# Kernel tuning notes

Hardware: AMD Instinct MI355X
Metric: run time of the kernel (lower is better)

Reference implementation:

```python
import jax, jax.numpy as jnp
import numpy as np

B, A, C = 64, 8732, 81


def setup_inputs() -> dict:
    key = jax.random.key(0)
    k1, k2, k3, k4, k5 = jax.random.split(key, 5)
    scores = jax.random.normal(k1, (B, A, C), dtype=jnp.float32)
    boxes = jax.random.normal(k2, (B, A, 4), dtype=jnp.float32)
    gt_labels = jax.random.randint(k3, (B, A), 0, C)
    gt_boxes = jax.random.normal(k4, (B, A, 4), dtype=jnp.float32)
    mask = jax.random.uniform(k5, (B, A)) < 0.02
    return {"scores": scores, "boxes": boxes, "gt_labels": gt_labels,
            "gt_boxes": gt_boxes, "mask": mask}


def reference(scores, boxes, gt_labels, gt_boxes, mask):
    dtype = scores.dtype
    maskf = mask.astype(dtype)
    pos_num = mask.sum(axis=-1, keepdims=True)          # [B,1] per-image positives
    N = jnp.maximum(1, mask.sum()).astype(dtype)        # max(1, total positives)

    # localization: smooth L1 (beta=1) summed over positive anchors
    d = boxes - gt_boxes
    ad = jnp.abs(d)
    sl1 = jnp.where(ad < 1.0, 0.5 * d * d, ad - 0.5)    # [B,A,4]
    loc_loss = (sl1.sum(axis=-1) * maskf).sum() / N

    # per-anchor cross entropy
    logp = jax.nn.log_softmax(scores, axis=-1)          # [B,A,C]
    c_loss = -jnp.take_along_axis(logp, gt_labels[..., None], axis=-1)[..., 0]  # [B,A]

    # hard negative mining: zero positives, rank by descending loss, keep top 3*pos_num
    conf_neg = jnp.where(mask, jnp.zeros((), dtype), c_loss)
    conf_idx = jnp.argsort(-conf_neg, axis=-1)          # descending sort indices
    rank = jnp.argsort(conf_idx, axis=-1)               # rank of each anchor
    neg_mask = rank < 3 * pos_num                       # [B,A]

    conf_loss = ((c_loss * maskf).sum() + (c_loss * neg_mask.astype(dtype)).sum()) / N
    total_loss = loc_loss + conf_loss
    return total_loss, loc_loss, conf_loss
```

## Files before the change

### kernel.cpp

```cpp
#include <hip/hip_runtime.h>
#include <math.h>

#define NB 64
#define NA 8732
#define NC 81
#define TOTAL (NB * NA)
#define APB 128
#define TPB 512
#define NBLK (TOTAL / APB)


__device__ __forceinline__ float quadsum(float x) {
    x += __int_as_float(__builtin_amdgcn_update_dpp(
        0, __float_as_int(x), 0xB1, 0xF, 0xF, true));
    x += __int_as_float(__builtin_amdgcn_update_dpp(
        0, __float_as_int(x), 0x4E, 0xF, 0xF, true));
    return x;
}

__device__ __forceinline__ void gload_lds16(const float4* g, float4* l) {
    __builtin_amdgcn_global_load_lds(
        (const __attribute__((address_space(1))) unsigned int*)g,
        (__attribute__((address_space(3))) unsigned int*)l,
        16, 0, 0);
}

__global__ __launch_bounds__(TPB) void main_kernel(
    const float* __restrict__ scores, const float* __restrict__ boxes,
    const int* __restrict__ gt_labels, const float* __restrict__ gt_boxes,
    const int* __restrict__ mask, float* __restrict__ conf_neg,
    float* __restrict__ block_loc, float* __restrict__ block_pcs)
{
    __shared__ float lds[APB * NC];
    __shared__ float wredl[8], wredp[8];
    const int tid  = threadIdx.x;
    const int lane = tid & 63;
    const int wid  = tid >> 6;
    const int base = blockIdx.x * APB;

    const float4* __restrict__ src = (const float4*)(scores + (size_t)base * NC);
    float4* dst = (float4*)lds;
    gload_lds16(src + tid,        dst + tid);
    gload_lds16(src + tid +  512, dst + tid +  512);
    gload_lds16(src + tid + 1024, dst + tid + 1024);
    gload_lds16(src + tid + 1536, dst + tid + 1536);
    gload_lds16(src + tid + 2048, dst + tid + 2048);
    if (tid < 32) gload_lds16(src + tid + 2560, dst + tid + 2560);

    float loc = 0.0f;
    if (tid < APB) {
        const int a = base + tid;
        if (mask[a]) {
            const float4 bx = *(const float4*)(boxes    + (size_t)a * 4);
            const float4 gb = *(const float4*)(gt_boxes + (size_t)a * 4);
            const float d0 = bx.x - gb.x, d1 = bx.y - gb.y;
            const float d2 = bx.z - gb.z, d3 = bx.w - gb.w;
            const float a0 = fabsf(d0), a1 = fabsf(d1), a2 = fabsf(d2), a3 = fabsf(d3);
            loc = (a0 < 1.f ? 0.5f * d0 * d0 : a0 - 0.5f)
                + (a1 < 1.f ? 0.5f * d1 * d1 : a1 - 0.5f)
                + (a2 < 1.f ? 0.5f * d2 * d2 : a2 - 0.5f)
                + (a3 < 1.f ? 0.5f * d3 * d3 : a3 - 0.5f);
        }
    }
    __syncthreads();

    const int al = tid >> 2;
    const int q  = tid & 3;
    const float* __restrict__ row = lds + al * NC;
    float e = 0.0f;
    #pragma unroll
    for (int j = 0; j < 20; ++j) e += __expf(row[q * 20 + j]);
    if (q == 3) e += __expf(row[80]);
    e = quadsum(e);

    float pcs = 0.0f;
    if (q == 0) {
        const int a = base + al;
        const int lab = gt_labels[a];
        const float c = __logf(e) - row[lab];
        const int m = mask[a];
        conf_neg[a] = m ? 0.f : c;
        pcs = m ? c : 0.f;
    }

    #pragma unroll
    for (int o = 32; o; o >>= 1) {
        loc += __shfl_down(loc, o);
        pcs += __shfl_down(pcs, o);
    }
    if (lane == 0) { wredl[wid] = loc; wredp[wid] = pcs; }
    __syncthreads();
    if (tid == 0) {
        float sl = 0.f, sp = 0.f;
        #pragma unroll
        for (int w = 0; w < 8; ++w) { sl += wredl[w]; sp += wredp[w]; }
        block_loc[blockIdx.x] = sl;
        block_pcs[blockIdx.x] = sp;
    }
}

__global__ __launch_bounds__(1024) void topk_kernel(
    const float* __restrict__ conf_neg, const int* __restrict__ mask,
    int* __restrict__ pos_count, float* __restrict__ accv)
{
    __shared__ unsigned sv[NA];
    __shared__ __align__(16) int whist[64][256];
    __shared__ int hist4[4][256];
    __shared__ int   redi[16];
    __shared__ float redf[16];
    __shared__ unsigned spfx;
    __shared__ int skr;
    __shared__ int sk;
    const int tid  = threadIdx.x;
    const int lane = tid & 63;
    const int wid  = tid >> 6;
    const int hid  = tid >> 4;
    const int b = blockIdx.x;
    const float* __restrict__ row  = conf_neg + (size_t)b * NA;
    const int*   __restrict__ mrow = mask     + (size_t)b * NA;

    int myc = 0;
    for (int i = tid; i < NA; i += 1024) {
        sv[i] = __float_as_uint(row[i]);
        myc += mrow[i];
    }
    #pragma unroll
    for (int o = 32; o; o >>= 1) myc += __shfl_down(myc, o);
    if (lane == 0) redi[wid] = myc;
    __syncthreads();
    if (tid == 0) {
        int p = 0;
        #pragma unroll
        for (int w = 0; w < 16; ++w) p += redi[w];
        pos_count[b] = p;
        int kk = 3 * p;
        if (kk > NA) kk = NA;
        sk = kk;
    }
    __syncthreads();
    int k = sk;
    if (k <= 0) {
        if (tid == 0) accv[b] = 0.0f;
        return;
    }

    unsigned prefix = 0u;
    int kr = k;
    for (int shift = 24; shift >= 0; shift -= 8) {
        int4* w4 = (int4*)whist;
        const int4 z = make_int4(0, 0, 0, 0);
        w4[tid] = z; w4[tid + 1024] = z; w4[tid + 2048] = z; w4[tid + 3072] = z;
        __syncthreads();

        const unsigned himask = (shift == 24) ? 0u : (0xFFFFFFFFu << (shift + 8));
        for (int i = tid; i < NA; i += 1024) {
            const unsigned v = sv[i];
            if ((v & himask) == prefix)
                atomicAdd(&whist[hid][(v >> shift) & 255], 1);
        }
        __syncthreads();

        {
            const int p = tid >> 8;
            const int bb = tid & 255;
            int s = 0;
            #pragma unroll
            for (int w = 0; w < 16; ++w) s += whist[(p << 4) + w][bb];
            hist4[p][bb] = s;
        }
        __syncthreads();

        if (wid == 0) {
            int h0, h1, h2, h3;
            {
                const int b0i = 4 * lane;
                h0 = hist4[0][b0i]     + hist4[1][b0i]     + hist4[2][b0i]     + hist4[3][b0i];
                h1 = hist4[0][b0i + 1] + hist4[1][b0i + 1] + hist4[2][b0i + 1] + hist4[3][b0i + 1];
                h2 = hist4[0][b0i + 2] + hist4[1][b0i + 2] + hist4[2][b0i + 2] + hist4[3][b0i + 2];
                h3 = hist4[0][b0i + 3] + hist4[1][b0i + 3] + hist4[2][b0i + 3] + hist4[3][b0i + 3];
            }
            const int s3 = h3, s2 = h2 + s3, s1 = h1 + s2, s0 = h0 + s1;
            int incl = s0;
            #pragma unroll
            for (int off = 1; off < 64; off <<= 1) {
                const int v = __shfl_down(incl, off);
                if (lane + off < 64) incl += v;
            }
            const int E = incl - s0;
            const int S0 = E + s0, S1 = E + s1, S2 = E + s2, S3 = E + s3;
            if (S0 >= kr && S1 < kr) { spfx = prefix | ((unsigned)(4 * lane)     << shift); skr = kr - S1; }
            else if (S1 >= kr && S2 < kr) { spfx = prefix | ((unsigned)(4 * lane + 1) << shift); skr = kr - S2; }
            else if (S2 >= kr && S3 < kr) { spfx = prefix | ((unsigned)(4 * lane + 2) << shift); skr = kr - S3; }
            else if (S3 >= kr && E  < kr) { spfx = prefix | ((unsigned)(4 * lane + 3) << shift); skr = kr - E;  }
        }
        __syncthreads();
        prefix = spfx;
        kr = skr;
    }

    float s = 0.0f; int cg = 0;
    for (int i = tid; i < NA; i += 1024) {
        const unsigned u = sv[i];
        if (u > prefix) { s += __uint_as_float(u); cg++; }
    }
    #pragma unroll
    for (int o = 32; o; o >>= 1) { s += __shfl_down(s, o); cg += __shfl_down(cg, o); }
    if ((tid & 63) == 0) { redf[wid] = s; redi[wid] = cg; }
    __syncthreads();
    if (tid == 0) {
        float ts = 0.f; int tc = 0;
        #pragma unroll
        for (int w = 0; w < 16; ++w) { ts += redf[w]; tc += redi[w]; }
        ts += (float)(k - tc) * __uint_as_float(prefix);
        accv[b] = ts;
    }
}

__global__ __launch_bounds__(1024) void final_kernel(
    const float* __restrict__ block_loc, const float* __restrict__ block_pcs,
    const int* __restrict__ pos_count, const float* __restrict__ accv,
    float* __restrict__ out)
{
    __shared__ float rl[16], rp[16];
    const int tid = threadIdx.x;
    const int wid = tid >> 6;
    float sl = 0.f, sp = 0.f;
    for (int i = tid; i < NBLK; i += 1024) { sl += block_loc[i]; sp += block_pcs[i]; }
    int   p  = (tid < NB) ? pos_count[tid] : 0;
    float sa = (tid < NB) ? accv[tid]      : 0.f;
    #pragma unroll
    for (int o = 32; o; o >>= 1) {
        sl += __shfl_down(sl, o);
        sp += __shfl_down(sp, o);
        p  += __shfl_down(p, o);
        sa += __shfl_down(sa, o);
    }
    if ((tid & 63) == 0) { rl[wid] = sl; rp[wid] = sp; }
    __syncthreads();
    if (tid == 0) {
        float tl = 0.f, tp = 0.f;
        #pragma unroll
        for (int w = 0; w < 16; ++w) { tl += rl[w]; tp += rp[w]; }
        const float N = fmaxf(1.0f, (float)p);
        const float loc  = tl / N;
        const float conf = (tp + sa) / N;
        out[0] = loc + conf;
        out[1] = loc;
        out[2] = conf;
    }
}

extern "C" void kernel_launch(void* const* d_in, const int* in_sizes, int n_in,
                              void* d_out, int out_size, void* d_ws, size_t ws_size,
                              hipStream_t stream) {
    const float* scores    = (const float*)d_in[0];
    const float* boxes     = (const float*)d_in[1];
    const int*   gt_labels = (const int*)d_in[2];
    const float* gt_boxes  = (const float*)d_in[3];
    const int*   mask      = (const int*)d_in[4];
    float* out = (float*)d_out;

    float* conf_neg  = (float*)d_ws;
    int*   pos_count = (int*)(conf_neg + TOTAL);
    float* accv      = (float*)(pos_count + NB);
    float* block_loc = accv + NB;
    float* block_pcs = block_loc + NBLK;

    hipLaunchKernelGGL(main_kernel, dim3(NBLK), dim3(TPB), 0, stream,
                       scores, boxes, gt_labels, gt_boxes, mask,
                       conf_neg, block_loc, block_pcs);
    hipLaunchKernelGGL(topk_kernel, dim3(NB), dim3(1024), 0, stream,
                       conf_neg, mask, pos_count, accv);
    hipLaunchKernelGGL(final_kernel, dim3(1), dim3(1024), 0, stream,
                       block_loc, block_pcs, pos_count, accv, out);
}
```

Before: 284.0 us.

## Fuse final reduction into topk via last-block counter and halve main tile

Removes the separate final_kernel launch. The last topk block to finish, detected with an atomic counter that main_kernel resets, now does the global reduction and writes the outputs. Also halves the anchors per block in main_kernel (64 anchors, 256 threads) with an occupancy hint of 7 blocks per CU, to raise concurrency in the memory-bound scores pass. This adds an atomic and threadfences, and the 7-block hint may constrain registers.

```diff
diff --git a/kernel.cpp b/kernel.cpp
--- a/kernel.cpp
+++ b/kernel.cpp
@@ -5,8 +5,8 @@
 #define NA 8732
 #define NC 81
 #define TOTAL (NB * NA)
-#define APB 128
-#define TPB 512
+#define APB 64
+#define TPB 256
 #define NBLK (TOTAL / APB)
 
 
@@ -25,27 +25,30 @@
         16, 0, 0);
 }
 
-__global__ __launch_bounds__(TPB) void main_kernel(
+__global__ __launch_bounds__(TPB, 7) void main_kernel(
     const float* __restrict__ scores, const float* __restrict__ boxes,
     const int* __restrict__ gt_labels, const float* __restrict__ gt_boxes,
     const int* __restrict__ mask, float* __restrict__ conf_neg,
-    float* __restrict__ block_loc, float* __restrict__ block_pcs)
+    float* __restrict__ block_loc, float* __restrict__ block_pcs,
+    int* __restrict__ done)
 {
-    __shared__ float lds[APB * NC];
-    __shared__ float wredl[8], wredp[8];
+    __shared__ float lds[APB * NC + 256];
+    __shared__ float wredl[4], wredp[4];
     const int tid  = threadIdx.x;
     const int lane = tid & 63;
     const int wid  = tid >> 6;
     const int base = blockIdx.x * APB;
 
+    if (blockIdx.x == 0 && tid == 0) *done = 0;
+
     const float4* __restrict__ src = (const float4*)(scores + (size_t)base * NC);
     float4* dst = (float4*)lds;
     gload_lds16(src + tid,        dst + tid);
+    gload_lds16(src + tid +  256, dst + tid +  256);
     gload_lds16(src + tid +  512, dst + tid +  512);
+    gload_lds16(src + tid +  768, dst + tid +  768);
     gload_lds16(src + tid + 1024, dst + tid + 1024);
-    gload_lds16(src + tid + 1536, dst + tid + 1536);
-    gload_lds16(src + tid + 2048, dst + tid + 2048);
-    if (tid < 32) gload_lds16(src + tid + 2560, dst + tid + 2560);
+    if (tid < 16) gload_lds16(src + tid + 1280, dst + tid + 1280);
 
     float loc = 0.0f;
     if (tid < APB) {
@@ -91,26 +94,27 @@
     if (lane == 0) { wredl[wid] = loc; wredp[wid] = pcs; }
     __syncthreads();
     if (tid == 0) {
-        float sl = 0.f, sp = 0.f;
-        #pragma unroll
-        for (int w = 0; w < 8; ++w) { sl += wredl[w]; sp += wredp[w]; }
-        block_loc[blockIdx.x] = sl;
-        block_pcs[blockIdx.x] = sp;
+        block_loc[blockIdx.x] = wredl[0] + wredl[1] + wredl[2] + wredl[3];
+        block_pcs[blockIdx.x] = wredp[0] + wredp[1] + wredp[2] + wredp[3];
     }
 }
 
 __global__ __launch_bounds__(1024) void topk_kernel(
     const float* __restrict__ conf_neg, const int* __restrict__ mask,
-    int* __restrict__ pos_count, float* __restrict__ accv)
+    int* __restrict__ pos_count, float* __restrict__ accv,
+    const float* __restrict__ block_loc, const float* __restrict__ block_pcs,
+    int* __restrict__ done, float* __restrict__ out)
 {
     __shared__ unsigned sv[NA];
     __shared__ __align__(16) int whist[64][256];
     __shared__ int hist4[4][256];
     __shared__ int   redi[16];
     __shared__ float redf[16];
+    __shared__ float rl[16], rp[16];
     __shared__ unsigned spfx;
     __shared__ int skr;
     __shared__ int sk;
+    __shared__ int lastflag;
     const int tid  = threadIdx.x;
     const int lane = tid & 63;
     const int wid  = tid >> 6;
@@ -138,110 +142,107 @@
         sk = kk;
     }
     __syncthreads();
-    int k = sk;
-    if (k <= 0) {
+    const int k = sk;
+
+    if (k > 0) {
+        unsigned prefix = 0u;
+        int kr = k;
+        for (int shift = 24; shift >= 0; shift -= 8) {
+            int4* w4 = (int4*)whist;
+            const int4 z = make_int4(0, 0, 0, 0);
+            w4[tid] = z; w4[tid + 1024] = z; w4[tid + 2048] = z; w4[tid + 3072] = z;
+            __syncthreads();
+
+            const unsigned himask = (shift == 24) ? 0u : (0xFFFFFFFFu << (shift + 8));
+            for (int i = tid; i < NA; i += 1024) {
+                const unsigned v = sv[i];
+                if ((v & himask) == prefix)
+                    atomicAdd(&whist[hid][(v >> shift) & 255], 1);
+            }
+            __syncthreads();
+
+            {
+                const int p = tid >> 8;
+                const int bb = tid & 255;
+                int s = 0;
+                #pragma unroll
+                for (int w = 0; w < 16; ++w) s += whist[(p << 4) + w][bb];
+                hist4[p][bb] = s;
+            }
+            __syncthreads();
+
+            if (wid == 0) {
+                int h0, h1, h2, h3;
+                {
+                    const int b0i = 4 * lane;
+                    h0 = hist4[0][b0i]     + hist4[1][b0i]     + hist4[2][b0i]     + hist4[3][b0i];
+                    h1 = hist4[0][b0i + 1] + hist4[1][b0i + 1] + hist4[2][b0i + 1] + hist4[3][b0i + 1];
+                    h2 = hist4[0][b0i + 2] + hist4[1][b0i + 2] + hist4[2][b0i + 2] + hist4[3][b0i + 2];
+                    h3 = hist4[0][b0i + 3] + hist4[1][b0i + 3] + hist4[2][b0i + 3] + hist4[3][b0i + 3];
+                }
+                const int s3 = h3, s2 = h2 + s3, s1 = h1 + s2, s0 = h0 + s1;
+                int incl = s0;
+                #pragma unroll
+                for (int off = 1; off < 64; off <<= 1) {
+                    const int v = __shfl_down(incl, off);
+                    if (lane + off < 64) incl += v;
+                }
+                const int E = incl - s0;
+                const int S0 = E + s0, S1 = E + s1, S2 = E + s2, S3 = E + s3;
+                if (S0 >= kr && S1 < kr) { spfx = prefix | ((unsigned)(4 * lane)     << shift); skr = kr - S1; }
+                else if (S1 >= kr && S2 < kr) { spfx = prefix | ((unsigned)(4 * lane + 1) << shift); skr = kr - S2; }
+                else if (S2 >= kr && S3 < kr) { spfx = prefix | ((unsigned)(4 * lane + 2) << shift); skr = kr - S3; }
+                else if (S3 >= kr && E  < kr) { spfx = prefix | ((unsigned)(4 * lane + 3) << shift); skr = kr - E;  }
+            }
+            __syncthreads();
+            prefix = spfx;
+            kr = skr;
+        }
+
+        float s = 0.0f; int cg = 0;
+        for (int i = tid; i < NA; i += 1024) {
+            const unsigned u = sv[i];
+            if (u > prefix) { s += __uint_as_float(u); cg++; }
+        }
+        #pragma unroll
+        for (int o = 32; o; o >>= 1) { s += __shfl_down(s, o); cg += __shfl_down(cg, o); }
+        if ((tid & 63) == 0) { redf[wid] = s; redi[wid] = cg; }
+        __syncthreads();
+        if (tid == 0) {
+            float ts = 0.f; int tc = 0;
+            #pragma unroll
+            for (int w = 0; w < 16; ++w) { ts += redf[w]; tc += redi[w]; }
+            ts += (float)(k - tc) * __uint_as_float(prefix);
+            accv[b] = ts;
+        }
+    } else {
         if (tid == 0) accv[b] = 0.0f;
-        return;
-    }
-
-    unsigned prefix = 0u;
-    int kr = k;
-    for (int shift = 24; shift >= 0; shift -= 8) {
-        int4* w4 = (int4*)whist;
-        const int4 z = make_int4(0, 0, 0, 0);
-        w4[tid] = z; w4[tid + 1024] = z; w4[tid + 2048] = z; w4[tid + 3072] = z;
-        __syncthreads();
-
-        const unsigned himask = (shift == 24) ? 0u : (0xFFFFFFFFu << (shift + 8));
-        for (int i = tid; i < NA; i += 1024) {
-            const unsigned v = sv[i];
-            if ((v & himask) == prefix)
-                atomicAdd(&whist[hid][(v >> shift) & 255], 1);
-        }
-        __syncthreads();
-
-        {
-            const int p = tid >> 8;
-            const int bb = tid & 255;
-            int s = 0;
-            #pragma unroll
-            for (int w = 0; w < 16; ++w) s += whist[(p << 4) + w][bb];
-            hist4[p][bb] = s;
-        }
-        __syncthreads();
-
-        if (wid == 0) {
-            int h0, h1, h2, h3;
-            {
-                const int b0i = 4 * lane;
-                h0 = hist4[0][b0i]     + hist4[1][b0i]     + hist4[2][b0i]     + hist4[3][b0i];
-                h1 = hist4[0][b0i + 1] + hist4[1][b0i + 1] + hist4[2][b0i + 1] + hist4[3][b0i + 1];
-                h2 = hist4[0][b0i + 2] + hist4[1][b0i + 2] + hist4[2][b0i + 2] + hist4[3][b0i + 2];
-                h3 = hist4[0][b0i + 3] + hist4[1][b0i + 3] + hist4[2][b0i + 3] + hist4[3][b0i + 3];
-            }
-            const int s3 = h3, s2 = h2 + s3, s1 = h1 + s2, s0 = h0 + s1;
-            int incl = s0;
-            #pragma unroll
-            for (int off = 1; off < 64; off <<= 1) {
-                const int v = __shfl_down(incl, off);
-                if (lane + off < 64) incl += v;
-            }
-            const int E = incl - s0;
-            const int S0 = E + s0, S1 = E + s1, S2 = E + s2, S3 = E + s3;
-            if (S0 >= kr && S1 < kr) { spfx = prefix | ((unsigned)(4 * lane)     << shift); skr = kr - S1; }
-            else if (S1 >= kr && S2 < kr) { spfx = prefix | ((unsigned)(4 * lane + 1) << shift); skr = kr - S2; }
-            else if (S2 >= kr && S3 < kr) { spfx = prefix | ((unsigned)(4 * lane + 2) << shift); skr = kr - S3; }
-            else if (S3 >= kr && E  < kr) { spfx = prefix | ((unsigned)(4 * lane + 3) << shift); skr = kr - E;  }
-        }
-        __syncthreads();
-        prefix = spfx;
-        kr = skr;
-    }
-
-    float s = 0.0f; int cg = 0;
-    for (int i = tid; i < NA; i += 1024) {
-        const unsigned u = sv[i];
-        if (u > prefix) { s += __uint_as_float(u); cg++; }
-    }
-    #pragma unroll
-    for (int o = 32; o; o >>= 1) { s += __shfl_down(s, o); cg += __shfl_down(cg, o); }
-    if ((tid & 63) == 0) { redf[wid] = s; redi[wid] = cg; }
-    __syncthreads();
-    if (tid == 0) {
-        float ts = 0.f; int tc = 0;
-        #pragma unroll
-        for (int w = 0; w < 16; ++w) { ts += redf[w]; tc += redi[w]; }
-        ts += (float)(k - tc) * __uint_as_float(prefix);
-        accv[b] = ts;
-    }
-}
-
-__global__ __launch_bounds__(1024) void final_kernel(
-    const float* __restrict__ block_loc, const float* __restrict__ block_pcs,
-    const int* __restrict__ pos_count, const float* __restrict__ accv,
-    float* __restrict__ out)
-{
-    __shared__ float rl[16], rp[16];
-    const int tid = threadIdx.x;
-    const int wid = tid >> 6;
+    }
+
+    __threadfence();
+    if (tid == 0) lastflag = (atomicAdd(done, 1) == NB - 1);
+    __syncthreads();
+    if (!lastflag) return;
+    __threadfence();
+
     float sl = 0.f, sp = 0.f;
     for (int i = tid; i < NBLK; i += 1024) { sl += block_loc[i]; sp += block_pcs[i]; }
-    int   p  = (tid < NB) ? pos_count[tid] : 0;
+    int   p2 = (tid < NB) ? pos_count[tid] : 0;
     float sa = (tid < NB) ? accv[tid]      : 0.f;
     #pragma unroll
     for (int o = 32; o; o >>= 1) {
         sl += __shfl_down(sl, o);
         sp += __shfl_down(sp, o);
-        p  += __shfl_down(p, o);
+        p2 += __shfl_down(p2, o);
         sa += __shfl_down(sa, o);
     }
-    if ((tid & 63) == 0) { rl[wid] = sl; rp[wid] = sp; }
+    if (lane == 0) { rl[wid] = sl; rp[wid] = sp; }
     __syncthreads();
     if (tid == 0) {
         float tl = 0.f, tp = 0.f;
         #pragma unroll
         for (int w = 0; w < 16; ++w) { tl += rl[w]; tp += rp[w]; }
-        const float N = fmaxf(1.0f, (float)p);
+        const float N = fmaxf(1.0f, (float)p2);
         const float loc  = tl / N;
         const float conf = (tp + sa) / N;
         out[0] = loc + conf;
@@ -265,12 +266,12 @@
     float* accv      = (float*)(pos_count + NB);
     float* block_loc = accv + NB;
     float* block_pcs = block_loc + NBLK;
+    int*   done      = (int*)(block_pcs + NBLK);
 
     hipLaunchKernelGGL(main_kernel, dim3(NBLK), dim3(TPB), 0, stream,
                        scores, boxes, gt_labels, gt_boxes, mask,
-                       conf_neg, block_loc, block_pcs);
+                       conf_neg, block_loc, block_pcs, done);
     hipLaunchKernelGGL(topk_kernel, dim3(NB), dim3(1024), 0, stream,
-                       conf_neg, mask, pos_count, accv);
-    hipLaunchKernelGGL(final_kernel, dim3(1), dim3(1024), 0, stream,
-                       block_loc, block_pcs, pos_count, accv, out);
-}
+                       conf_neg, mask, pos_count, accv,
+                       block_loc, block_pcs, done, out);
+}
```

New measurement: 303.8 us. 1.07x slower.
